# Optimization experiments

Hardware: AMD Instinct MI355X
Metric: run time of the kernel (lower is better)

The kernel has to match this reference:

```python
import jax, jax.numpy as jnp
import numpy as np

L, DIRS, H, I, B, T = 2, 2, 512, 1024, 64, 1024


def _gru_dir(x_seq, h0, w_ih, w_hh, b_ih, b_hh, reverse):
    """Run one GRU direction. x_seq: (B,T,in), h0: (B,H). Returns (out (B,T,H), h_T (B,H))."""
    # Precompute input projections for all timesteps: (T,B,3H)
    gi = jnp.einsum('bti,gi->tbg', x_seq, w_ih) + b_ih

    def step(h, gi_t):
        gh = h @ w_hh.T + b_hh                      # (B,3H)
        i_r, i_z, i_n = jnp.split(gi_t, 3, axis=-1)
        h_r, h_z, h_n = jnp.split(gh, 3, axis=-1)
        r = jax.nn.sigmoid(i_r + h_r)
        z = jax.nn.sigmoid(i_z + h_z)
        n = jnp.tanh(i_n + r * h_n)
        h_new = (1.0 - z) * n + z * h
        return h_new, h_new

    h_T, out = jax.lax.scan(step, h0, gi, reverse=reverse)
    return out.transpose(1, 0, 2), h_T            # (B,T,H), (B,H)


def setup_inputs() -> dict:
    key = jax.random.key(0)
    ks = jax.random.split(key, 6)
    s = 1.0 / np.sqrt(H)  # PyTorch-style init scale, avoids gate saturation
    return {
        'x':    jax.random.normal(ks[0], (B, T, I), jnp.float32),
        'h0':   jax.random.normal(ks[1], (L * DIRS, B, H), jnp.float32) * s,
        'w_ih': jax.random.normal(ks[2], (L, DIRS, 3 * H, I), jnp.float32) * s,
        'w_hh': jax.random.normal(ks[3], (L, DIRS, 3 * H, H), jnp.float32) * s,
        'b_ih': jax.random.normal(ks[4], (L, DIRS, 3 * H), jnp.float32) * s,
        'b_hh': jax.random.normal(ks[5], (L, DIRS, 3 * H), jnp.float32) * s,
    }


def reference(x, h0, w_ih, w_hh, b_ih, b_hh):
    layer_in = x
    h_finals = []
    for l in range(L):  # small fixed loop over structurally distinct layers
        out_f, hT_f = _gru_dir(layer_in, h0[2 * l],     w_ih[l, 0], w_hh[l, 0], b_ih[l, 0], b_hh[l, 0], reverse=False)
        out_b, hT_b = _gru_dir(layer_in, h0[2 * l + 1], w_ih[l, 1], w_hh[l, 1], b_ih[l, 1], b_hh[l, 1], reverse=True)
        layer_in = jnp.concatenate([out_f, out_b], axis=-1)  # (B,T,2H)
        h_finals.extend([hT_f, hT_b])
    h_n = jnp.stack(h_finals, axis=0)  # (L*2, B, H), PyTorch ordering
    return layer_in, h_n
```

## Files before the change

kernel.cpp:

```cpp
#include <hip/hip_runtime.h>
#include <stdint.h>
#include <stdio.h>

#define TL 1024
#define BB 64
#define HH 512
#define II 1024
#define NL 2
#define BT_ (BB*TL)
#define G3_ 1536
#define N2_ 3072

typedef _Float16 h8 __attribute__((ext_vector_type(8)));
typedef _Float16 h4 __attribute__((ext_vector_type(4)));
typedef _Float16 h2 __attribute__((ext_vector_type(2)));
typedef float    f4 __attribute__((ext_vector_type(4)));
typedef unsigned int u4 __attribute__((ext_vector_type(4)));

__global__ void cvt_f2h(const float* __restrict__ src, _Float16* __restrict__ dst, size_t n4) {
  size_t i = (size_t)blockIdx.x*blockDim.x + threadIdx.x;
  size_t stride = (size_t)gridDim.x*blockDim.x;
  for (; i < n4; i += stride) {
    f4 v = ((const f4*)src)[i];
    h4 o;
    o[0] = (_Float16)v[0]; o[1] = (_Float16)v[1];
    o[2] = (_Float16)v[2]; o[3] = (_Float16)v[3];
    ((h4*)dst)[i] = o;
  }
}

#define LDA 40
__launch_bounds__(256)
__global__ void gemm_gi(const _Float16* __restrict__ A, const _Float16* __restrict__ Bw,
                        const float* __restrict__ bias, _Float16* __restrict__ gi)
{
  const int bn = blockIdx.x, bm = blockIdx.y;
  const int tid = threadIdx.x;
  const int wave = tid >> 6, lane = tid & 63;
  const int wm = wave >> 1, wn = wave & 1;
  const int lo = lane & 15, hi = lane >> 4;
  __shared__ _Float16 As[128*LDA];
  __shared__ _Float16 Bs[128*LDA];
  f4 acc[4][4] = {};
  const int r0 = tid >> 2, c0 = (tid & 3)*8;
  const _Float16* Ag = A + (size_t)(bm*128)*II;
  const _Float16* Bg = Bw + (size_t)(bn*128)*II;
  u4 a0 = *(const u4*)(Ag + (size_t)r0*II + c0);
  u4 a1 = *(const u4*)(Ag + (size_t)(64+r0)*II + c0);
  u4 b0 = *(const u4*)(Bg + (size_t)r0*II + c0);
  u4 b1 = *(const u4*)(Bg + (size_t)(64+r0)*II + c0);
  for (int kt = 0; kt < 32; ++kt) {
    __syncthreads();
    *(u4*)&As[r0*LDA + c0] = a0;
    *(u4*)&As[(64+r0)*LDA + c0] = a1;
    *(u4*)&Bs[r0*LDA + c0] = b0;
    *(u4*)&Bs[(64+r0)*LDA + c0] = b1;
    if (kt+1 < 32) {
      const int off = (kt+1)*32 + c0;
      a0 = *(const u4*)(Ag + (size_t)r0*II + off);
      a1 = *(const u4*)(Ag + (size_t)(64+r0)*II + off);
      b0 = *(const u4*)(Bg + (size_t)r0*II + off);
      b1 = *(const u4*)(Bg + (size_t)(64+r0)*II + off);
    }
    __syncthreads();
    h8 af[4], bf[4];
    #pragma unroll
    for (int i = 0; i < 4; ++i)
      af[i] = *(const h8*)&As[(wm*64 + i*16 + lo)*LDA + hi*8];
    #pragma unroll
    for (int j = 0; j < 4; ++j)
      bf[j] = *(const h8*)&Bs[(wn*64 + j*16 + lo)*LDA + hi*8];
    #pragma unroll
    for (int i = 0; i < 4; ++i)
      #pragma unroll
      for (int j = 0; j < 4; ++j)
        acc[i][j] = __builtin_amdgcn_mfma_f32_16x16x32_f16(af[i], bf[j], acc[i][j], 0, 0, 0);
  }
  const int nbase = bn*128 + wn*64;
  const int mbase = bm*128 + wm*64;
  #pragma unroll
  for (int j = 0; j < 4; ++j) {
    int n = nbase + j*16 + lo;
    int dir = (n >= G3_) ? 1 : 0;
    int row = n - dir*G3_;
    float bs = bias[n];
    #pragma unroll
    for (int i = 0; i < 4; ++i) {
      int m0 = mbase + i*16 + hi*4;
      #pragma unroll
      for (int v = 0; v < 4; ++v)
        gi[((size_t)dir*BT_ + (size_t)(m0+v))*G3_ + row] = (_Float16)(acc[i][j][v] + bs);
    }
  }
}

#define LDW 520
__launch_bounds__(384, 1)
__global__ void gru_layer(const _Float16* __restrict__ gi,
                          const _Float16* __restrict__ whh,
                          const float* __restrict__ bhh,
                          const float* __restrict__ h0,
                          _Float16* __restrict__ h_buf,
                          unsigned* __restrict__ cnt,
                          _Float16* __restrict__ out_mid,
                          float* __restrict__ out_fin,
                          float* __restrict__ hn_out,
                          int layer)
{
  const int bid = blockIdx.x;
  const int gg = bid & 7, d = gg & 1, g = gg >> 1;
  const int member = bid >> 3;
  const int j0 = member * 32, b0 = g * 16;
  const int tid = threadIdx.x;
  const int wave = tid >> 6, lane = tid & 63, lo = lane & 15, hi = lane >> 4;
  const int gate = wave >> 1, jh = wave & 1;

  __shared__ _Float16 wlds[3][32][LDW];
  __shared__ _Float16 hlds[16][LDW];
  __shared__ float    ghlds[3][32][17];

  const _Float16* wsrc = whh + (size_t)d*G3_*HH;
  #pragma unroll
  for (int it = 0; it < 16; ++it) {
    int idx = it*384 + tid;
    int row = idx >> 6;
    int c8 = (idx & 63) * 8;
    int gt = row >> 5, jj = row & 31;
    u4 v = *(const u4*)(wsrc + (size_t)(gt*HH + j0 + jj)*HH + c8);
    *(u4*)&wlds[gt][jj][c8] = v;
  }

  unsigned* mycnt = cnt + gg*32;
  const int ejp = tid & 15;
  const int eb  = tid >> 4;
  const bool ew = (tid < 256);
  const int ejA = j0 + 2*ejp;

  float hj[2];
  float bhr[2], bhz[2], bhn[2];

  if (ew) {
    #pragma unroll
    for (int u = 0; u < 2; ++u) {
      bhr[u] = bhh[(size_t)d*G3_ + 0*HH + ejA + u];
      bhz[u] = bhh[(size_t)d*G3_ + 1*HH + ejA + u];
      bhn[u] = bhh[(size_t)d*G3_ + 2*HH + ejA + u];
      hj[u]  = h0[((size_t)(2*layer + d)*BB + b0 + eb)*HH + ejA + u];
    }
    h2 p; p[0] = (_Float16)hj[0]; p[1] = (_Float16)hj[1];
    unsigned pu = __builtin_bit_cast(unsigned, p);
    unsigned old = __hip_atomic_exchange(
        (unsigned*)(h_buf + (((size_t)d*2 + 0)*BB + b0 + eb)*HH + ejA),
        pu, __ATOMIC_RELAXED, __HIP_MEMORY_SCOPE_AGENT);
    asm volatile("" :: "v"(old));
  }
  asm volatile("s_waitcnt vmcnt(0)" ::: "memory");
  __syncthreads();
  if (tid == 0)
    __hip_atomic_fetch_add(mycnt, 1u, __ATOMIC_RELAXED, __HIP_MEMORY_SCOPE_AGENT);

  for (int s = 0; s < TL; ++s) {
    const int t = d ? (TL-1 - s) : s;
    const int rpar = s & 1, wpar = rpar ^ 1;
    unsigned giR = 0, giZ = 0, giN = 0;
    if (ew) {
      const _Float16* p = gi + ((size_t)d*BT_ + (size_t)(b0 + eb)*TL + t)*(size_t)G3_ + ejA;
      giR = *(const unsigned*)(p);
      giZ = *(const unsigned*)(p + HH);
      giN = *(const unsigned*)(p + 2*HH);
    }
    if (tid == 0) {
      unsigned target = 16u*(unsigned)(s + 1);
      while (__hip_atomic_load(mycnt, __ATOMIC_RELAXED, __HIP_MEMORY_SCOPE_AGENT) < target) {}
    }
    __syncthreads();
    {
      const uint64_t* src = (const uint64_t*)(h_buf + (((size_t)d*2 + rpar)*BB + b0)*HH);
      #pragma unroll
      for (int it = 0; it < 6; ++it) {
        int idx = it*384 + tid;
        if (idx < 2048) {
          int b = idx >> 7, jq = idx & 127;
          uint64_t v = __hip_atomic_load(src + (size_t)b*128 + jq,
                                         __ATOMIC_RELAXED, __HIP_MEMORY_SCOPE_AGENT);
          *(uint64_t*)&hlds[b][jq*4] = v;
        }
      }
    }
    __syncthreads();
    f4 acc = {0.f, 0.f, 0.f, 0.f};
    #pragma unroll
    for (int kk = 0; kk < 16; ++kk) {
      h8 af = *(const h8*)&hlds[lo][kk*32 + hi*8];
      h8 bf = *(const h8*)&wlds[gate][jh*16 + lo][kk*32 + hi*8];
      acc = __builtin_amdgcn_mfma_f32_16x16x32_f16(af, bf, acc, 0, 0, 0);
    }
    #pragma unroll
    for (int v = 0; v < 4; ++v)
      ghlds[gate][jh*16 + lo][hi*4 + v] = acc[v];
    __syncthreads();
    if (ew) {
      h2 pR = __builtin_bit_cast(h2, giR);
      h2 pZ = __builtin_bit_cast(h2, giZ);
      h2 pN = __builtin_bit_cast(h2, giN);
      h2 hnew;
      float hv[2];
      #pragma unroll
      for (int u = 0; u < 2; ++u) {
        float ir = (float)pR[u], iz = (float)pZ[u], inn = (float)pN[u];
        float hr = ghlds[0][2*ejp+u][eb] + bhr[u];
        float hz = ghlds[1][2*ejp+u][eb] + bhz[u];
        float hn = ghlds[2][2*ejp+u][eb] + bhn[u];
        float rr = 1.f/(1.f + __expf(-(ir + hr)));
        float zz = 1.f/(1.f + __expf(-(iz + hz)));
        float xx = inn + rr*hn;
        float nn = 1.f - 2.f/(__expf(2.f*xx) + 1.f);
        float h  = (1.f - zz)*nn + zz*hj[u];
        hj[u] = h;
        hnew[u] = (_Float16)h;
        hv[u] = h;
      }
      unsigned hu = __builtin_bit_cast(unsigned, hnew);
      unsigned old = __hip_atomic_exchange(
          (unsigned*)(h_buf + (((size_t)d*2 + wpar)*BB + b0 + eb)*HH + ejA),
          hu, __ATOMIC_RELAXED, __HIP_MEMORY_SCOPE_AGENT);
      asm volatile("" :: "v"(old));
      if (out_mid) {
        *(unsigned*)(out_mid + ((size_t)(b0+eb)*TL + t)*(size_t)(2*HH) + d*HH + ejA) = hu;
      } else {
        out_fin[((size_t)(b0+eb)*TL + t)*(size_t)(2*HH) + d*HH + ejA]     = hv[0];
        out_fin[((size_t)(b0+eb)*TL + t)*(size_t)(2*HH) + d*HH + ejA + 1] = hv[1];
      }
    }
    asm volatile("s_waitcnt vmcnt(0)" ::: "memory");
    __syncthreads();
    if (tid == 0)
      __hip_atomic_fetch_add(mycnt, 1u, __ATOMIC_RELAXED, __HIP_MEMORY_SCOPE_AGENT);
  }
  if (ew) {
    #pragma unroll
    for (int u = 0; u < 2; ++u)
      hn_out[((size_t)(2*layer + d)*BB + b0 + eb)*HH + ejA + u] = hj[u];
  }
}

extern "C" void kernel_launch(void* const* d_in, const int* in_sizes, int n_in,
                              void* d_out, int out_size, void* d_ws, size_t ws_size,
                              hipStream_t stream) {
  (void)in_sizes; (void)n_in; (void)out_size;
  const float* x   = (const float*)d_in[0];
  const float* h0  = (const float*)d_in[1];
  const float* wih = (const float*)d_in[2];
  const float* whh = (const float*)d_in[3];
  const float* bih = (const float*)d_in[4];
  const float* bhh = (const float*)d_in[5];
  float* out = (float*)d_out;

  char* ws = (char*)d_ws;
  size_t off = 0;
  auto alloc = [&](size_t bytes) {
    char* p = ws + off;
    off += (bytes + 255) & ~(size_t)255;
    return p;
  };
  _Float16* x16   = (_Float16*)alloc((size_t)BT_*II*2);
  _Float16* mid16 = (_Float16*)alloc((size_t)BT_*II*2);
  _Float16* gi16  = (_Float16*)alloc((size_t)2*BT_*G3_*2);
  _Float16* wih16 = (_Float16*)alloc((size_t)NL*N2_*II*2);
  _Float16* whh16 = (_Float16*)alloc((size_t)NL*N2_*HH*2);
  _Float16* hbuf  = (_Float16*)alloc((size_t)2*2*BB*HH*2);
  unsigned* cnt   = (unsigned*)alloc((size_t)16*32*4);
  if (off > ws_size) {
    fprintf(stderr, "kernel_launch: workspace too small: need %zu have %zu\n", off, ws_size);
    return;
  }

  hipMemsetAsync(cnt, 0, (size_t)16*32*4, stream);
  cvt_f2h<<<2048, 256, 0, stream>>>(x,   x16,   (size_t)BT_*II/4);
  cvt_f2h<<<512,  256, 0, stream>>>(wih, wih16, (size_t)NL*N2_*II/4);
  cvt_f2h<<<512,  256, 0, stream>>>(whh, whh16, (size_t)NL*N2_*HH/4);

  float* hn = out + (size_t)BT_*II;

  gemm_gi<<<dim3(24, 512), 256, 0, stream>>>(x16, wih16, bih, gi16);
  gru_layer<<<128, 384, 0, stream>>>(gi16, whh16, bhh, h0, hbuf, cnt,
                                     mid16, nullptr, hn, 0);
  gemm_gi<<<dim3(24, 512), 256, 0, stream>>>(mid16, wih16 + (size_t)N2_*II, bih + N2_, gi16);
  gru_layer<<<128, 384, 0, stream>>>(gi16, whh16 + (size_t)N2_*HH, bhh + N2_, h0, hbuf, cnt + 8*32,
                                     nullptr, out, hn, 1);
}
```

Baseline: 8.701 ms.

## Replace counter barrier with step-tagged hidden-state entries for inter-block sync

The shared arrival counter and the spin-wait before each timestep are removed. Each fp16 pair of the hidden state is now stored in a 64-bit word that also carries its timestep tag. Readers poll the tagged words directly, copy them into LDS, and retry until every tag is current. This drops the vmcnt drain, the extra barrier and the atomic increment from each step. In exchange, each poll reads twice as many bytes and may repeat loads while other blocks lag. The final fp32 output stores are also merged into one vector store.

```diff
diff --git a/kernel.cpp b/kernel.cpp
--- a/kernel.cpp
+++ b/kernel.cpp
@@ -16,6 +16,7 @@
 typedef _Float16 h2 __attribute__((ext_vector_type(2)));
 typedef float    f4 __attribute__((ext_vector_type(4)));
 typedef unsigned int u4 __attribute__((ext_vector_type(4)));
+typedef unsigned int u2v __attribute__((ext_vector_type(2)));
 
 __global__ void cvt_f2h(const float* __restrict__ src, _Float16* __restrict__ dst, size_t n4) {
   size_t i = (size_t)blockIdx.x*blockDim.x + threadIdx.x;
@@ -100,8 +101,7 @@
                           const _Float16* __restrict__ whh,
                           const float* __restrict__ bhh,
                           const float* __restrict__ h0,
-                          _Float16* __restrict__ h_buf,
-                          unsigned* __restrict__ cnt,
+                          unsigned long long* __restrict__ tagh,
                           _Float16* __restrict__ out_mid,
                           float* __restrict__ out_fin,
                           float* __restrict__ hn_out,
@@ -118,6 +118,7 @@
   __shared__ _Float16 wlds[3][32][LDW];
   __shared__ _Float16 hlds[16][LDW];
   __shared__ float    ghlds[3][32][17];
+  __shared__ unsigned wok[8];
 
   const _Float16* wsrc = whh + (size_t)d*G3_*HH;
   #pragma unroll
@@ -130,11 +131,12 @@
     *(u4*)&wlds[gt][jj][c8] = v;
   }
 
-  unsigned* mycnt = cnt + gg*32;
   const int ejp = tid & 15;
   const int eb  = tid >> 4;
   const bool ew = (tid < 256);
   const int ejA = j0 + 2*ejp;
+
+  unsigned long long* Tb = tagh + (size_t)d*2*BB*256;
 
   float hj[2];
   float bhr[2], bhz[2], bhn[2];
@@ -148,20 +150,16 @@
       hj[u]  = h0[((size_t)(2*layer + d)*BB + b0 + eb)*HH + ejA + u];
     }
     h2 p; p[0] = (_Float16)hj[0]; p[1] = (_Float16)hj[1];
-    unsigned pu = __builtin_bit_cast(unsigned, p);
-    unsigned old = __hip_atomic_exchange(
-        (unsigned*)(h_buf + (((size_t)d*2 + 0)*BB + b0 + eb)*HH + ejA),
-        pu, __ATOMIC_RELAXED, __HIP_MEMORY_SCOPE_AGENT);
-    asm volatile("" :: "v"(old));
-  }
-  asm volatile("s_waitcnt vmcnt(0)" ::: "memory");
+    unsigned long long ent = (unsigned long long)__builtin_bit_cast(unsigned, p) | (1ull << 32);
+    unsigned long long* ptr = Tb + (size_t)0*BB*256 + (size_t)(b0 + eb)*256 + (member*16 + ejp);
+    __hip_atomic_store(ptr, ent, __ATOMIC_RELAXED, __HIP_MEMORY_SCOPE_AGENT);
+  }
   __syncthreads();
-  if (tid == 0)
-    __hip_atomic_fetch_add(mycnt, 1u, __ATOMIC_RELAXED, __HIP_MEMORY_SCOPE_AGENT);
 
   for (int s = 0; s < TL; ++s) {
     const int t = d ? (TL-1 - s) : s;
     const int rpar = s & 1, wpar = rpar ^ 1;
+    const unsigned tgt = (unsigned)(s + 1);
     unsigned giR = 0, giZ = 0, giN = 0;
     if (ew) {
       const _Float16* p = gi + ((size_t)d*BT_ + (size_t)(b0 + eb)*TL + t)*(size_t)G3_ + ejA;
@@ -169,25 +167,38 @@
       giZ = *(const unsigned*)(p + HH);
       giN = *(const unsigned*)(p + 2*HH);
     }
-    if (tid == 0) {
-      unsigned target = 16u*(unsigned)(s + 1);
-      while (__hip_atomic_load(mycnt, __ATOMIC_RELAXED, __HIP_MEMORY_SCOPE_AGENT) < target) {}
-    }
-    __syncthreads();
     {
-      const uint64_t* src = (const uint64_t*)(h_buf + (((size_t)d*2 + rpar)*BB + b0)*HH);
-      #pragma unroll
-      for (int it = 0; it < 6; ++it) {
-        int idx = it*384 + tid;
-        if (idx < 2048) {
-          int b = idx >> 7, jq = idx & 127;
-          uint64_t v = __hip_atomic_load(src + (size_t)b*128 + jq,
-                                         __ATOMIC_RELAXED, __HIP_MEMORY_SCOPE_AGENT);
-          *(uint64_t*)&hlds[b][jq*4] = v;
+      const unsigned long long* Trd = Tb + (size_t)rpar*BB*256;
+      for (;;) {
+        unsigned long long E0[6], E1[6];
+        #pragma unroll
+        for (int it = 0; it < 6; ++it) {
+          int idx = it*384 + tid;
+          if (idx < 2048) {
+            const unsigned long long* pa = Trd + (size_t)(b0 + (idx >> 7))*256 + (idx & 127)*2;
+            E0[it] = __hip_atomic_load(pa,     __ATOMIC_RELAXED, __HIP_MEMORY_SCOPE_AGENT);
+            E1[it] = __hip_atomic_load(pa + 1, __ATOMIC_RELAXED, __HIP_MEMORY_SCOPE_AGENT);
+          }
         }
+        unsigned okm = 1u;
+        #pragma unroll
+        for (int it = 0; it < 6; ++it) {
+          int idx = it*384 + tid;
+          if (idx < 2048) {
+            okm &= (unsigned)((E0[it] >> 32) >= tgt) & (unsigned)((E1[it] >> 32) >= tgt);
+            int b = idx >> 7, j4 = (idx & 127)*4;
+            u2v dv; dv[0] = (unsigned)E0[it]; dv[1] = (unsigned)E1[it];
+            *(u2v*)&hlds[b][j4] = dv;
+          }
+        }
+        unsigned long long bal = __ballot(okm != 0u);
+        if (lane == 0) wok[wave] = (bal == ~0ull) ? 1u : 0u;
+        __syncthreads();
+        unsigned allok = wok[0] & wok[1] & wok[2] & wok[3] & wok[4] & wok[5];
+        if (allok) break;
+        __syncthreads();
       }
     }
-    __syncthreads();
     f4 acc = {0.f, 0.f, 0.f, 0.f};
     #pragma unroll
     for (int kk = 0; kk < 16; ++kk) {
@@ -203,8 +214,7 @@
       h2 pR = __builtin_bit_cast(h2, giR);
       h2 pZ = __builtin_bit_cast(h2, giZ);
       h2 pN = __builtin_bit_cast(h2, giN);
-      h2 hnew;
-      float hv[2];
+      h2 hnew; float hv[2];
       #pragma unroll
       for (int u = 0; u < 2; ++u) {
         float ir = (float)pR[u], iz = (float)pZ[u], inn = (float)pN[u];
@@ -216,26 +226,19 @@
         float xx = inn + rr*hn;
         float nn = 1.f - 2.f/(__expf(2.f*xx) + 1.f);
         float h  = (1.f - zz)*nn + zz*hj[u];
-        hj[u] = h;
-        hnew[u] = (_Float16)h;
-        hv[u] = h;
+        hj[u] = h; hnew[u] = (_Float16)h; hv[u] = h;
       }
       unsigned hu = __builtin_bit_cast(unsigned, hnew);
-      unsigned old = __hip_atomic_exchange(
-          (unsigned*)(h_buf + (((size_t)d*2 + wpar)*BB + b0 + eb)*HH + ejA),
-          hu, __ATOMIC_RELAXED, __HIP_MEMORY_SCOPE_AGENT);
-      asm volatile("" :: "v"(old));
+      unsigned long long ent = (unsigned long long)hu | ((unsigned long long)(s + 2) << 32);
+      unsigned long long* ptr = Tb + (size_t)wpar*BB*256 + (size_t)(b0 + eb)*256 + (member*16 + ejp);
+      __hip_atomic_store(ptr, ent, __ATOMIC_RELAXED, __HIP_MEMORY_SCOPE_AGENT);
       if (out_mid) {
         *(unsigned*)(out_mid + ((size_t)(b0+eb)*TL + t)*(size_t)(2*HH) + d*HH + ejA) = hu;
       } else {
-        out_fin[((size_t)(b0+eb)*TL + t)*(size_t)(2*HH) + d*HH + ejA]     = hv[0];
-        out_fin[((size_t)(b0+eb)*TL + t)*(size_t)(2*HH) + d*HH + ejA + 1] = hv[1];
+        u2v ov; ov[0] = __builtin_bit_cast(unsigned, hv[0]); ov[1] = __builtin_bit_cast(unsigned, hv[1]);
+        *(u2v*)(out_fin + ((size_t)(b0+eb)*TL + t)*(size_t)(2*HH) + d*HH + ejA) = ov;
       }
     }
-    asm volatile("s_waitcnt vmcnt(0)" ::: "memory");
-    __syncthreads();
-    if (tid == 0)
-      __hip_atomic_fetch_add(mycnt, 1u, __ATOMIC_RELAXED, __HIP_MEMORY_SCOPE_AGENT);
   }
   if (ew) {
     #pragma unroll
@@ -268,14 +271,13 @@
   _Float16* gi16  = (_Float16*)alloc((size_t)2*BT_*G3_*2);
   _Float16* wih16 = (_Float16*)alloc((size_t)NL*N2_*II*2);
   _Float16* whh16 = (_Float16*)alloc((size_t)NL*N2_*HH*2);
-  _Float16* hbuf  = (_Float16*)alloc((size_t)2*2*BB*HH*2);
-  unsigned* cnt   = (unsigned*)alloc((size_t)16*32*4);
+  unsigned long long* tagh = (unsigned long long*)alloc((size_t)NL*2*2*BB*256*8);
   if (off > ws_size) {
     fprintf(stderr, "kernel_launch: workspace too small: need %zu have %zu\n", off, ws_size);
     return;
   }
 
-  hipMemsetAsync(cnt, 0, (size_t)16*32*4, stream);
+  hipMemsetAsync(tagh, 0, (size_t)NL*2*2*BB*256*8, stream);
   cvt_f2h<<<2048, 256, 0, stream>>>(x,   x16,   (size_t)BT_*II/4);
   cvt_f2h<<<512,  256, 0, stream>>>(wih, wih16, (size_t)NL*N2_*II/4);
   cvt_f2h<<<512,  256, 0, stream>>>(whh, whh16, (size_t)NL*N2_*HH/4);
@@ -283,9 +285,9 @@
   float* hn = out + (size_t)BT_*II;
 
   gemm_gi<<<dim3(24, 512), 256, 0, stream>>>(x16, wih16, bih, gi16);
-  gru_layer<<<128, 384, 0, stream>>>(gi16, whh16, bhh, h0, hbuf, cnt,
+  gru_layer<<<128, 384, 0, stream>>>(gi16, whh16, bhh, h0, tagh,
                                      mid16, nullptr, hn, 0);
   gemm_gi<<<dim3(24, 512), 256, 0, stream>>>(mid16, wih16 + (size_t)N2_*II, bih + N2_, gi16);
-  gru_layer<<<128, 384, 0, stream>>>(gi16, whh16 + (size_t)N2_*HH, bhh + N2_, h0, hbuf, cnt + 8*32,
-                                     nullptr, out, hn, 1);
-}
+  gru_layer<<<128, 384, 0, stream>>>(gi16, whh16 + (size_t)N2_*HH, bhh + N2_, h0,
+                                     tagh + (size_t)2*2*BB*256, nullptr, out, hn, 1);
+}
```

Measured after the change: 8.284 ms. 4.8% less time.
